# Kernel tuning notes

Hardware: AMD Instinct MI355X
Metric: run time of the kernel (lower is better)

Reference implementation:

```python
import jax, jax.numpy as jnp
import numpy as np

C = 256
LN_EPS = 1e-5
LEAKY_SLOPE = 0.01

def _layernorm(t, g, b):
    mu = jnp.mean(t, axis=-1, keepdims=True)
    var = jnp.mean((t - mu) ** 2, axis=-1, keepdims=True)
    return (t - mu) * jax.lax.rsqrt(var + LN_EPS) * g + b

def setup_inputs() -> dict:
    key = jax.random.key(0)
    ks = jax.random.split(key, 16)
    b, d, h, w = 4, 4096, 64, 64
    s = lambda n: 1.0 / np.sqrt(n)
    return {
        "x": jax.random.normal(ks[0], (b, 1, d), jnp.float32),
        "y": jax.random.normal(ks[1], (b, C, h, w), jnp.float32),
        "q_w": jax.random.normal(ks[2], (C, C), jnp.float32) * s(C),
        "q_b": jnp.zeros((C,), jnp.float32),
        "dw_w": jax.random.normal(ks[3], (C,), jnp.float32),
        "dw_b": jnp.zeros((C,), jnp.float32),
        "kv_w1": jax.random.normal(ks[4], (1, C // 2), jnp.float32),
        "kv_b1": jnp.zeros((C // 2,), jnp.float32),
        "ln1_g": jnp.ones((C // 2,), jnp.float32),
        "ln1_b": jnp.zeros((C // 2,), jnp.float32),
        "kv_w2": jax.random.normal(ks[5], (C // 2, C), jnp.float32) * s(C // 2),
        "kv_b2": jnp.zeros((C,), jnp.float32),
        "ln2_g": jnp.ones((C,), jnp.float32),
        "ln2_b": jnp.zeros((C,), jnp.float32),
        "kv_w3": jax.random.normal(ks[6], (C, C), jnp.float32) * s(C),
        "kv_b3": jnp.zeros((C,), jnp.float32),
        "ln3_g": jnp.ones((C,), jnp.float32),
        "ln3_b": jnp.zeros((C,), jnp.float32),
        "kv_w4": jax.random.normal(ks[7], (C, 2 * C), jnp.float32) * s(C),
        "kv_b4": jnp.zeros((2 * C,), jnp.float32),
        "proj_w": jax.random.normal(ks[8], (C, C), jnp.float32) * s(C),
        "proj_b": jnp.zeros((C,), jnp.float32),
    }

def reference(x, y, q_w, q_b, dw_w, dw_b, kv_w1, kv_b1, ln1_g, ln1_b,
              kv_w2, kv_b2, ln2_g, ln2_b, kv_w3, kv_b3, ln3_g, ln3_b,
              kv_w4, kv_b4, proj_w, proj_b):
    b, c, h, w = y.shape
    # x: [b, 1, d] -> [b, d, 1]; MLP kv-generator lifts each scalar to 2c channels
    t = jnp.swapaxes(x, 1, 2)  # [b, d, 1]
    t = jax.nn.leaky_relu(_layernorm(t @ kv_w1 + kv_b1, ln1_g, ln1_b), LEAKY_SLOPE)
    t = jax.nn.leaky_relu(_layernorm(t @ kv_w2 + kv_b2, ln2_g, ln2_b), LEAKY_SLOPE)
    t = jax.nn.leaky_relu(_layernorm(t @ kv_w3 + kv_b3, ln3_g, ln3_b), LEAKY_SLOPE)
    t = jax.nn.silu(t @ kv_w4 + kv_b4)  # [b, d, 2c]
    k, v = jnp.split(t, 2, axis=-1)  # each [b, d, c]
    k = jnp.swapaxes(k, 1, 2)  # [b, c, d]
    # q = dwconv1x1(conv1x1(y)): 1x1 conv is a channel matmul; depthwise 1x1 is per-channel affine
    q = jnp.einsum('bchw,oc->bohw', y, q_w) + q_b[None, :, None, None]
    q = q * dw_w[None, :, None, None] + dw_b[None, :, None, None]
    q = q.reshape(b, c, h * w).transpose(0, 2, 1)  # [b, hw, c]
    scores = jnp.einsum('bic,bcd->bid', q, k) * (float(c) ** -0.5)  # [b, hw, d]
    attn = jax.nn.softmax(scores, axis=2)
    h_ = jnp.einsum('bid,bdc->bic', attn, v)  # [b, hw, c]
    h_ = h_.transpose(0, 2, 1).reshape(b, c, h, w)
    h_ = jnp.einsum('bchw,oc->bohw', h_, proj_w) + proj_b[None, :, None, None]
    return y + h_
```

## Files before the change

### kernel.cpp

```cpp
#include <hip/hip_runtime.h>
#include <cstdint>
#include <cstddef>

using bf16   = __bf16;
using bf16x8 = __bf16 __attribute__((ext_vector_type(8)));
using f32x4  = float  __attribute__((ext_vector_type(4)));
using u16    = unsigned short;
using ushort8 = __attribute__((ext_vector_type(8))) unsigned short;

#define MFMA16(a, b, c) __builtin_amdgcn_mfma_f32_16x16x32_bf16(a, b, c, 0, 0, 0)

__device__ __forceinline__ u16 f2bf(float f) {
  union { float f; unsigned u; } v; v.f = f;
  unsigned r = v.u + 0x7fffu + ((v.u >> 16) & 1u);
  return (u16)(r >> 16);
}
__device__ __forceinline__ u16 bfc(float f) {
  union { float f; unsigned u; } v; v.f = f;
  return (u16)((v.u + 0x8000u) >> 16);
}
__device__ __forceinline__ float b2f(u16 h) {
  union { unsigned u; float f; } v; v.u = ((unsigned)h) << 16; return v.f;
}
__device__ __forceinline__ bf16x8 ldb8(const u16* p) { return *(const bf16x8*)p; }
__device__ __forceinline__ float red_sum16(float v) {
  v += __shfl_xor(v, 1, 64); v += __shfl_xor(v, 2, 64);
  v += __shfl_xor(v, 4, 64); v += __shfl_xor(v, 8, 64);
  return v;
}
__device__ __forceinline__ void gll16(const u16* g, u16* l) {
  __builtin_amdgcn_global_load_lds(
      (const __attribute__((address_space(1))) void*)g,
      (__attribute__((address_space(3))) void*)l, 16, 0, 0);
}

#define QSCALE 0.09016844005556021f

__global__ void k_prep(const float* __restrict__ kv_w2, const float* __restrict__ kv_w3,
                       const float* __restrict__ kv_w4, const float* __restrict__ q_w,
                       const float* __restrict__ proj_w,
                       u16* __restrict__ Wt2, u16* __restrict__ Wt3, u16* __restrict__ Wt4,
                       u16* __restrict__ Qw, u16* __restrict__ Pww) {
  int idx = blockIdx.x * 256 + threadIdx.x;
  if (idx < 32768) {
    int n = idx >> 7, k = idx & 127;
    Wt2[idx] = f2bf(kv_w2[k * 256 + n]);
  } else if (idx < 98304) {
    int j = idx - 32768, n = j >> 8, k = j & 255;
    Wt3[j] = f2bf(kv_w3[k * 256 + n]);
  } else if (idx < 229376) {
    int j = idx - 98304, n = j >> 8, k = j & 255;
    Wt4[j] = f2bf(kv_w4[k * 512 + n]);
  } else if (idx < 294912) {
    int j = idx - 229376;
    Qw[j] = f2bf(q_w[j]);
  } else if (idx < 360448) {
    int j = idx - 294912;
    Pww[j] = f2bf(proj_w[j]);
  }
}

__device__ __forceinline__ void ln_store(f32x4* acc, const float* __restrict__ bias,
    const float* __restrict__ g, const float* __restrict__ bb, u16* act,
    int w, int quad, int l16) {
  #pragma unroll
  for (int f = 0; f < 16; ++f) {
    float bv = bias[f * 16 + l16];
    acc[f][0] += bv; acc[f][1] += bv; acc[f][2] += bv; acc[f][3] += bv;
  }
  #pragma unroll
  for (int r = 0; r < 4; ++r) {
    float s = 0;
    #pragma unroll
    for (int f = 0; f < 16; ++f) s += acc[f][r];
    s = red_sum16(s);
    float mu = s * (1.f / 256.f);
    float vv = 0;
    #pragma unroll
    for (int f = 0; f < 16; ++f) { float d = acc[f][r] - mu; vv += d * d; }
    vv = red_sum16(vv);
    float inv = rsqrtf(vv * (1.f / 256.f) + 1e-5f);
    int rl = w * 16 + quad * 4 + r;
    #pragma unroll
    for (int f = 0; f < 16; ++f) {
      int col = f * 16 + l16;
      float o = (acc[f][r] - mu) * inv * g[col] + bb[col];
      o = o > 0.f ? o : 0.01f * o;
      act[rl * 264 + col] = f2bf(o);
    }
  }
}

template<int K>
__device__ __forceinline__ void mlp_layer(u16* act, u16* sW, const u16* __restrict__ Wt,
    const float* __restrict__ bias, const float* __restrict__ g, const float* __restrict__ bb,
    int tid, int w, int quad, int l16) {
  bf16x8 af[K / 32];
  #pragma unroll
  for (int kk = 0; kk < K / 32; ++kk) af[kk] = ldb8(act + (w * 16 + l16) * 264 + kk * 32 + quad * 8);
  f32x4 z = {0.f, 0.f, 0.f, 0.f};
  f32x4 acc[16];
  #pragma unroll
  for (int f = 0; f < 16; ++f) acc[f] = z;
  for (int nc = 0; nc < 8; ++nc) {
    __syncthreads();
    #pragma unroll
    for (int p = 0; p < K / 64; ++p) {
      int q = p * 256 + tid; int row = q / (K / 8), c8 = q % (K / 8);
      *(uint4*)(sW + row * 264 + c8 * 8) = *(const uint4*)(Wt + (size_t)(nc * 32 + row) * K + c8 * 8);
    }
    __syncthreads();
    #pragma unroll
    for (int nb = 0; nb < 2; ++nb) {
      int f = nc * 2 + nb;
      #pragma unroll
      for (int kk = 0; kk < K / 32; ++kk)
        acc[f] = MFMA16(af[kk], ldb8(sW + (nb * 16 + l16) * 264 + kk * 32 + quad * 8), acc[f]);
    }
  }
  ln_store(acc, bias, g, bb, act, w, quad, l16);
  __syncthreads();
}

__device__ __forceinline__ void mlp_layer4(u16* act, u16* sW, const u16* __restrict__ Wt4,
    const float* __restrict__ bias4, u16* __restrict__ Kt, u16* __restrict__ Vt,
    int i0, int tid, int w, int quad, int l16) {
  bf16x8 af[8];
  #pragma unroll
  for (int kk = 0; kk < 8; ++kk) af[kk] = ldb8(act + (w * 16 + l16) * 264 + kk * 32 + quad * 8);
  f32x4 z = {0.f, 0.f, 0.f, 0.f};
  for (int h = 0; h < 2; ++h) {
    f32x4 acc[16];
    #pragma unroll
    for (int f = 0; f < 16; ++f) acc[f] = z;
    for (int nc = 0; nc < 8; ++nc) {
      __syncthreads();
      #pragma unroll
      for (int p = 0; p < 4; ++p) {
        int q = p * 256 + tid; int row = q >> 5, c8 = q & 31;
        *(uint4*)(sW + row * 264 + c8 * 8) =
            *(const uint4*)(Wt4 + (size_t)(h * 256 + nc * 32 + row) * 256 + c8 * 8);
      }
      __syncthreads();
      #pragma unroll
      for (int nb = 0; nb < 2; ++nb) {
        int f = nc * 2 + nb;
        #pragma unroll
        for (int kk = 0; kk < 8; ++kk)
          acc[f] = MFMA16(af[kk], ldb8(sW + (nb * 16 + l16) * 264 + kk * 32 + quad * 8), acc[f]);
      }
    }
    #pragma unroll
    for (int f = 0; f < 16; ++f) {
      int col = f * 16 + l16;
      float bv = bias4[h * 256 + col];
      if (h == 0) {
        int chunk = f * 2 + (l16 >> 3), co = col & 7;
        #pragma unroll
        for (int r = 0; r < 4; ++r) {
          int rowg = i0 + w * 16 + quad * 4 + r;
          float v = acc[f][r] + bv;
          v = v / (1.f + __expf(-v));
          int chs = (chunk + (rowg & 31)) & 31;
          Kt[(size_t)rowg * 256 + chs * 8 + co] = f2bf(v);
        }
      } else {
        int rowg0 = i0 + w * 16 + quad * 4;
        int bb2 = rowg0 >> 12, d0 = rowg0 & 4095;
        int dd = d0 & 31, qd = dd >> 3;
        int chs = (qd + (col & 3) + ((col >> 2) & 3)) & 3;
        ushort4 u;
        #pragma unroll
        for (int r = 0; r < 4; ++r) {
          float v = acc[f][r] + bv;
          v = v / (1.f + __expf(-v));
          ((u16*)&u)[r] = f2bf(v);
        }
        size_t off = ((size_t)(bb2 * 128 + (d0 >> 5)) * 8192) + col * 32 + chs * 8 + (dd & 7);
        *(ushort4*)(Vt + off) = u;
      }
    }
  }
}

__global__ __launch_bounds__(256, 2) void k_fused(
    const float* __restrict__ x, const float* __restrict__ w1, const float* __restrict__ bias1,
    const float* __restrict__ g1, const float* __restrict__ bb1,
    const u16* __restrict__ Wt2, const float* __restrict__ bias2,
    const float* __restrict__ g2, const float* __restrict__ bb2,
    const u16* __restrict__ Wt3, const float* __restrict__ bias3,
    const float* __restrict__ g3, const float* __restrict__ bb3,
    const u16* __restrict__ Wt4, const float* __restrict__ bias4,
    const float* __restrict__ y, const u16* __restrict__ Qw,
    const float* __restrict__ qb, const float* __restrict__ dww, const float* __restrict__ dwb,
    u16* __restrict__ Kt, u16* __restrict__ Vt, u16* __restrict__ Qb) {
  __shared__ __align__(16) u16 smem[25344];
  int tid = threadIdx.x, w = tid >> 6, lane = tid & 63, quad = lane >> 4, l16 = lane & 15;

  if (blockIdx.x < 256) {
    u16* act = smem;
    u16* sW  = smem + 16896;
    int i0 = blockIdx.x * 64;
    {
      int rloc = w * 16 + (lane >> 2);
      int c0 = (lane & 3) * 32;
      float xv = x[i0 + rloc];
      float t[32];
      float s = 0.f;
      #pragma unroll
      for (int j = 0; j < 32; ++j) { t[j] = xv * w1[c0 + j] + bias1[c0 + j]; s += t[j]; }
      s += __shfl_xor(s, 1, 64); s += __shfl_xor(s, 2, 64);
      float mu = s * (1.f / 128.f);
      float vv = 0.f;
      #pragma unroll
      for (int j = 0; j < 32; ++j) { float d = t[j] - mu; vv += d * d; }
      vv += __shfl_xor(vv, 1, 64); vv += __shfl_xor(vv, 2, 64);
      float inv = rsqrtf(vv * (1.f / 128.f) + 1e-5f);
      #pragma unroll
      for (int jo = 0; jo < 4; ++jo) {
        ushort8 pk;
        #pragma unroll
        for (int e = 0; e < 8; ++e) {
          int j = jo * 8 + e;
          float o = (t[j] - mu) * inv * g1[c0 + j] + bb1[c0 + j];
          o = o > 0.f ? o : 0.01f * o;
          pk[e] = f2bf(o);
        }
        *(ushort8*)(act + rloc * 264 + c0 + jo * 8) = pk;
      }
    }
    __syncthreads();
    mlp_layer<128>(act, sW, Wt2, bias2, g2, bb2, tid, w, quad, l16);
    mlp_layer<256>(act, sW, Wt3, bias3, g3, bb3, tid, w, quad, l16);
    mlp_layer4(act, sW, Wt4, bias4, Kt, Vt, i0, tid, w, quad, l16);
    return;
  }

  u16* sY = smem;
  u16* sB = smem + 4608;
  int t = blockIdx.x - 256;
  int b = t >> 6, i0 = (t & 63) * 64;
  f32x4 z = {0.f, 0.f, 0.f, 0.f};
  f32x4 acc[16];
  #pragma unroll
  for (int f = 0; f < 16; ++f) acc[f] = z;
  for (int kc = 0; kc < 4; ++kc) {
    if (kc) __syncthreads();
    {
      int cl = tid >> 4;
      int il = (tid & 15) * 4;
      #pragma unroll
      for (int p = 0; p < 4; ++p) {
        int c = kc * 64 + p * 16 + cl;
        float4 v = *(const float4*)(y + ((size_t)(b * 256 + c)) * 4096 + i0 + il);
        sY[(il + 0) * 72 + p * 16 + cl] = f2bf(v.x);
        sY[(il + 1) * 72 + p * 16 + cl] = f2bf(v.y);
        sY[(il + 2) * 72 + p * 16 + cl] = f2bf(v.z);
        sY[(il + 3) * 72 + p * 16 + cl] = f2bf(v.w);
      }
    }
    #pragma unroll
    for (int p = 0; p < 8; ++p) {
      int q = p * 256 + tid; int row = q >> 3, k8 = q & 7;
      *(uint4*)(sB + row * 72 + k8 * 8) = *(const uint4*)(Qw + (size_t)row * 256 + kc * 64 + k8 * 8);
    }
    __syncthreads();
    #pragma unroll
    for (int kk = 0; kk < 2; ++kk) {
      bf16x8 af = ldb8(sY + (w * 16 + l16) * 72 + kk * 32 + quad * 8);
      #pragma unroll
      for (int f = 0; f < 16; ++f) {
        bf16x8 bfr = ldb8(sB + (f * 16 + l16) * 72 + kk * 32 + quad * 8);
        acc[f] = MFMA16(af, bfr, acc[f]);
      }
    }
  }
  #pragma unroll
  for (int f = 0; f < 16; ++f) {
    int col = f * 16 + l16;
    float q0 = qb[col], sc = dww[col], dB = dwb[col];
    #pragma unroll
    for (int r = 0; r < 4; ++r) {
      int rowg = i0 + w * 16 + quad * 4 + r;
      float v = ((acc[f][r] + q0) * sc + dB) * QSCALE;
      Qb[((size_t)(b * 4096 + rowg)) * 256 + col] = f2bf(v);
    }
  }
}

__global__ __launch_bounds__(256, 2) void k_attn(const u16* __restrict__ Qb, const u16* __restrict__ Kt,
    const u16* __restrict__ Vt, u16* __restrict__ Op, float* __restrict__ Ol) {
  __shared__ __align__(16) u16 smem[37888];
  int tid = threadIdx.x, w = tid >> 6, lane = tid & 63, quad = lane >> 4, l16 = lane & 15;
  int b = blockIdx.x & 3, kh = (blockIdx.x >> 2) & 3, qt = blockIdx.x >> 4;
  int i0 = qt * 128 + w * 32;

  bf16x8 qf[2][8];
  {
    const u16* qrow = Qb + ((size_t)(b * 4096 + i0 + l16)) * 256 + quad * 8;
    #pragma unroll
    for (int kk = 0; kk < 8; ++kk) {
      qf[0][kk] = ldb8(qrow + kk * 32);
      qf[1][kk] = ldb8(qrow + 16 * 256 + kk * 32);
    }
  }
  f32x4 z = {0.f, 0.f, 0.f, 0.f};
  f32x4 oacc[2][16];
  #pragma unroll
  for (int sub = 0; sub < 2; ++sub)
    #pragma unroll
    for (int f = 0; f < 16; ++f) oacc[sub][f] = z;
  float l4[2][4] = {{0.f, 0.f, 0.f, 0.f}, {0.f, 0.f, 0.f, 0.f}};

  u16* sPw = smem + 32768 + w * 1280;
  int wp = w & 1;
  const u16* gSrc = ((w < 2) ? Kt : Vt) + ((size_t)(b * 128 + kh * 32) * 8192) + wp * 4096 + lane * 8;
  u16* lBase = smem + ((w < 2) ? 0 : 8192) + wp * 4096 + lane * 8;

  #pragma unroll
  for (int i = 0; i < 8; ++i) gll16(gSrc + i * 512, lBase + i * 512);
  gSrc += 8192;

  #pragma unroll 1
  for (int kt = 0; kt < 32; ++kt) {
    int buf = kt & 1;
    const u16* sK = smem + buf * 16384;
    const u16* sV = sK + 8192;
    asm volatile("s_waitcnt vmcnt(0)" ::: "memory");
    __syncthreads();
    if (kt < 31) {
      u16* dst = lBase + (buf ^ 1) * 16384;
      #pragma unroll
      for (int i = 0; i < 8; ++i) gll16(gSrc + i * 512, dst + i * 512);
      gSrc += 8192;
    }
    f32x4 s00 = z, s01 = z, s10 = z, s11 = z;
    #pragma unroll
    for (int kk = 0; kk < 8; ++kk) {
      int ch0 = (kk * 4 + quad + l16) & 31;
      int ch1 = (ch0 + 16) & 31;
      bf16x8 k0 = ldb8(sK + l16 * 256 + ch0 * 8);
      bf16x8 k1 = ldb8(sK + (16 + l16) * 256 + ch1 * 8);
      s00 = MFMA16(qf[0][kk], k0, s00);
      s01 = MFMA16(qf[0][kk], k1, s01);
      s10 = MFMA16(qf[1][kk], k0, s10);
      s11 = MFMA16(qf[1][kk], k1, s11);
    }
    #pragma unroll
    for (int r = 0; r < 4; ++r) {
      float p0 = exp2f(s00[r]);
      float p1 = exp2f(s01[r]);
      float p2 = exp2f(s10[r]);
      float p3 = exp2f(s11[r]);
      l4[0][r] += p0 + p1;
      l4[1][r] += p2 + p3;
      int row0 = (quad * 4 + r) * 40;
      sPw[row0 + l16]            = bfc(p0);
      sPw[row0 + 16 + l16]       = bfc(p1);
      sPw[640 + row0 + l16]      = bfc(p2);
      sPw[640 + row0 + 16 + l16] = bfc(p3);
    }
    asm volatile("s_waitcnt lgkmcnt(0)" ::: "memory");
    bf16x8 pf0 = ldb8(sPw + l16 * 40 + quad * 8);
    bf16x8 pf1 = ldb8(sPw + 640 + l16 * 40 + quad * 8);
    #pragma unroll
    for (int f = 0; f < 16; ++f) {
      int c = f * 16 + l16;
      int chs = (quad + (c & 3) + ((c >> 2) & 3)) & 3;
      bf16x8 vf = ldb8(sV + c * 32 + chs * 8);
      oacc[0][f] = MFMA16(pf0, vf, oacc[0][f]);
      oacc[1][f] = MFMA16(pf1, vf, oacc[1][f]);
    }
  }
  #pragma unroll
  for (int sub = 0; sub < 2; ++sub)
    #pragma unroll
    for (int r = 0; r < 4; ++r) l4[sub][r] = red_sum16(l4[sub][r]);
  #pragma unroll
  for (int sub = 0; sub < 2; ++sub)
    #pragma unroll
    for (int r = 0; r < 4; ++r) {
      size_t gr = (size_t)kh * 16384 + b * 4096 + i0 + sub * 16 + quad * 4 + r;
      u16* orow = Op + gr * 256;
      #pragma unroll
      for (int f = 0; f < 16; ++f) orow[f * 16 + l16] = f2bf(oacc[sub][f][r]);
      if (l16 == 0) Ol[gr] = l4[sub][r];
    }
}

__global__ __launch_bounds__(256) void k_proj(const u16* __restrict__ Op, const float* __restrict__ Ol,
    const u16* __restrict__ Pw, const float* __restrict__ pb, const float* __restrict__ y,
    float* __restrict__ out) {
  __shared__ u16 sA[64 * 136];
  __shared__ u16 sB[64 * 136];
  __shared__ float sW[64];
  int tid = threadIdx.x, w = tid >> 6, lane = tid & 63, quad = lane >> 4, l16 = lane & 15;
  int i0 = blockIdx.x * 64, o0 = blockIdx.y * 64, b = blockIdx.z;
  if (tid < 64) {
    size_t gr = (size_t)b * 4096 + i0 + tid;
    float L = Ol[gr] + Ol[gr + 16384] + Ol[gr + 32768] + Ol[gr + 49152];
    sW[tid] = 1.f / L;
  }
  __syncthreads();
  f32x4 z = {0.f, 0.f, 0.f, 0.f};
  f32x4 acc[4] = {z, z, z, z};
  for (int kc = 0; kc < 2; ++kc) {
    if (kc) __syncthreads();
    #pragma unroll
    for (int p = 0; p < 4; ++p) {
      int q = p * 256 + tid; int row = q >> 4, c8 = q & 15;
      *(uint4*)(sA + row * 136 + c8 * 8) = *(const uint4*)(Pw + ((size_t)(o0 + row)) * 256 + kc * 128 + c8 * 8);
      size_t gr = (size_t)b * 4096 + i0 + row;
      const u16* hp = Op + gr * 256 + kc * 128 + c8 * 8;
      uint4 u0 = *(const uint4*)(hp);
      uint4 u1 = *(const uint4*)(hp + 4194304);
      uint4 u2 = *(const uint4*)(hp + 8388608);
      uint4 u3 = *(const uint4*)(hp + 12582912);
      float wr = sW[row];
      const u16* p0 = (const u16*)&u0; const u16* p1 = (const u16*)&u1;
      const u16* p2 = (const u16*)&u2; const u16* p3 = (const u16*)&u3;
      ushort8 ov;
      #pragma unroll
      for (int e = 0; e < 8; ++e) {
        float v = (b2f(p0[e]) + b2f(p1[e]) + b2f(p2[e]) + b2f(p3[e])) * wr;
        ov[e] = f2bf(v);
      }
      *(ushort8*)(sB + row * 136 + c8 * 8) = ov;
    }
    __syncthreads();
    #pragma unroll
    for (int kk = 0; kk < 4; ++kk) {
      bf16x8 af = ldb8(sA + (w * 16 + l16) * 136 + kk * 32 + quad * 8);
      #pragma unroll
      for (int nb = 0; nb < 4; ++nb) {
        bf16x8 bfr = ldb8(sB + (nb * 16 + l16) * 136 + kk * 32 + quad * 8);
        acc[nb] = MFMA16(af, bfr, acc[nb]);
      }
    }
  }
  #pragma unroll
  for (int nb = 0; nb < 4; ++nb) {
    #pragma unroll
    for (int r = 0; r < 4; ++r) {
      int og = o0 + w * 16 + quad * 4 + r;
      size_t idx = ((size_t)(b * 256 + og)) * 4096 + i0 + nb * 16 + l16;
      out[idx] = y[idx] + acc[nb][r] + pb[og];
    }
  }
}

extern "C" void kernel_launch(void* const* d_in, const int* in_sizes, int n_in,
                              void* d_out, int out_size, void* d_ws, size_t ws_size,
                              hipStream_t stream) {
  (void)in_sizes; (void)n_in; (void)out_size; (void)ws_size;
  const float* x     = (const float*)d_in[0];
  const float* y     = (const float*)d_in[1];
  const float* q_w   = (const float*)d_in[2];
  const float* q_b   = (const float*)d_in[3];
  const float* dw_w  = (const float*)d_in[4];
  const float* dw_b  = (const float*)d_in[5];
  const float* kv_w1 = (const float*)d_in[6];
  const float* kv_b1 = (const float*)d_in[7];
  const float* ln1_g = (const float*)d_in[8];
  const float* ln1_b = (const float*)d_in[9];
  const float* kv_w2 = (const float*)d_in[10];
  const float* kv_b2 = (const float*)d_in[11];
  const float* ln2_g = (const float*)d_in[12];
  const float* ln2_b = (const float*)d_in[13];
  const float* kv_w3 = (const float*)d_in[14];
  const float* kv_b3 = (const float*)d_in[15];
  const float* ln3_g = (const float*)d_in[16];
  const float* ln3_b = (const float*)d_in[17];
  const float* kv_w4 = (const float*)d_in[18];
  const float* kv_b4 = (const float*)d_in[19];
  const float* proj_w = (const float*)d_in[20];
  const float* proj_b = (const float*)d_in[21];
  float* out = (float*)d_out;
  unsigned char* ws = (unsigned char*)d_ws;

  u16* Wt2 = (u16*)(ws + 0);
  u16* Wt3 = (u16*)(ws + 65536);
  u16* Wt4 = (u16*)(ws + 196608);
  u16* Qw  = (u16*)(ws + 458752);
  u16* Pww = (u16*)(ws + 589824);
  u16* Qb  = (u16*)(ws + 9437184);
  u16* Kt  = (u16*)(ws + 17825792);
  u16* Vt  = (u16*)(ws + 26214400);
  u16* Op  = (u16*)(ws + 34603008);
  float* Ol = (float*)(ws + 68157440);

  k_prep<<<1408, 256, 0, stream>>>(kv_w2, kv_w3, kv_w4, q_w, proj_w, Wt2, Wt3, Wt4, Qw, Pww);
  k_fused<<<512, 256, 0, stream>>>(x, kv_w1, kv_b1, ln1_g, ln1_b,
                                   Wt2, kv_b2, ln2_g, ln2_b,
                                   Wt3, kv_b3, ln3_g, ln3_b,
                                   Wt4, kv_b4,
                                   y, Qw, q_b, dw_w, dw_b,
                                   Kt, Vt, Qb);
  k_attn<<<512, 256, 0, stream>>>(Qb, Kt, Vt, Op, Ol);
  k_proj<<<dim3(64, 4, 4), 256, 0, stream>>>(Op, Ol, Pww, proj_b, y, out);
}
```

Measured before the change: 269.1 us.

## Make KV-MLP layers wave-local with direct global weight loads; pad P staging

The KV-generator MLP in k_fused now gives each wave its own 16-row activation tile in LDS and reads weight fragments straight from global memory (L2-cached) into MFMA operands. This removes the block-wide __syncthreads and the cooperative LDS staging of weight chunks. The row-level LayerNorm reductions are remapped to match. Separately, the attention kernel's P staging buffer gets a per-row skew to reduce LDS bank conflicts. The trade-off is more global and L2 weight traffic per wave and higher load latency in exchange for no barriers.

```diff
diff --git a/kernel.cpp b/kernel.cpp
--- a/kernel.cpp
+++ b/kernel.cpp
@@ -60,9 +60,24 @@
   }
 }
 
-__device__ __forceinline__ void ln_store(f32x4* acc, const float* __restrict__ bias,
-    const float* __restrict__ g, const float* __restrict__ bb, u16* act,
-    int w, int quad, int l16) {
+template<int K>
+__device__ __forceinline__ void wave_layer(u16* act, const u16* __restrict__ Wt,
+    const float* __restrict__ bias, const float* __restrict__ g, const float* __restrict__ bb,
+    int quad, int l16) {
+  bf16x8 af[K / 32];
+  #pragma unroll
+  for (int kk = 0; kk < K / 32; ++kk) af[kk] = ldb8(act + l16 * 264 + kk * 32 + quad * 8);
+  f32x4 z = {0.f, 0.f, 0.f, 0.f};
+  f32x4 acc[16];
+  #pragma unroll
+  for (int f = 0; f < 16; ++f) acc[f] = z;
+  #pragma unroll
+  for (int nb = 0; nb < 16; ++nb) {
+    const u16* wrow = Wt + (size_t)(nb * 16 + l16) * K + quad * 8;
+    #pragma unroll
+    for (int kk = 0; kk < K / 32; ++kk)
+      acc[nb] = MFMA16(af[kk], ldb8(wrow + kk * 32), acc[nb]);
+  }
   #pragma unroll
   for (int f = 0; f < 16; ++f) {
     float bv = bias[f * 16 + l16];
@@ -80,7 +95,7 @@
     for (int f = 0; f < 16; ++f) { float d = acc[f][r] - mu; vv += d * d; }
     vv = red_sum16(vv);
     float inv = rsqrtf(vv * (1.f / 256.f) + 1e-5f);
-    int rl = w * 16 + quad * 4 + r;
+    int rl = quad * 4 + r;
     #pragma unroll
     for (int f = 0; f < 16; ++f) {
       int col = f * 16 + l16;
@@ -89,98 +104,7 @@
       act[rl * 264 + col] = f2bf(o);
     }
   }
-}
-
-template<int K>
-__device__ __forceinline__ void mlp_layer(u16* act, u16* sW, const u16* __restrict__ Wt,
-    const float* __restrict__ bias, const float* __restrict__ g, const float* __restrict__ bb,
-    int tid, int w, int quad, int l16) {
-  bf16x8 af[K / 32];
-  #pragma unroll
-  for (int kk = 0; kk < K / 32; ++kk) af[kk] = ldb8(act + (w * 16 + l16) * 264 + kk * 32 + quad * 8);
-  f32x4 z = {0.f, 0.f, 0.f, 0.f};
-  f32x4 acc[16];
-  #pragma unroll
-  for (int f = 0; f < 16; ++f) acc[f] = z;
-  for (int nc = 0; nc < 8; ++nc) {
-    __syncthreads();
-    #pragma unroll
-    for (int p = 0; p < K / 64; ++p) {
-      int q = p * 256 + tid; int row = q / (K / 8), c8 = q % (K / 8);
-      *(uint4*)(sW + row * 264 + c8 * 8) = *(const uint4*)(Wt + (size_t)(nc * 32 + row) * K + c8 * 8);
-    }
-    __syncthreads();
-    #pragma unroll
-    for (int nb = 0; nb < 2; ++nb) {
-      int f = nc * 2 + nb;
-      #pragma unroll
-      for (int kk = 0; kk < K / 32; ++kk)
-        acc[f] = MFMA16(af[kk], ldb8(sW + (nb * 16 + l16) * 264 + kk * 32 + quad * 8), acc[f]);
-    }
-  }
-  ln_store(acc, bias, g, bb, act, w, quad, l16);
-  __syncthreads();
-}
-
-__device__ __forceinline__ void mlp_layer4(u16* act, u16* sW, const u16* __restrict__ Wt4,
-    const float* __restrict__ bias4, u16* __restrict__ Kt, u16* __restrict__ Vt,
-    int i0, int tid, int w, int quad, int l16) {
-  bf16x8 af[8];
-  #pragma unroll
-  for (int kk = 0; kk < 8; ++kk) af[kk] = ldb8(act + (w * 16 + l16) * 264 + kk * 32 + quad * 8);
-  f32x4 z = {0.f, 0.f, 0.f, 0.f};
-  for (int h = 0; h < 2; ++h) {
-    f32x4 acc[16];
-    #pragma unroll
-    for (int f = 0; f < 16; ++f) acc[f] = z;
-    for (int nc = 0; nc < 8; ++nc) {
-      __syncthreads();
-      #pragma unroll
-      for (int p = 0; p < 4; ++p) {
-        int q = p * 256 + tid; int row = q >> 5, c8 = q & 31;
-        *(uint4*)(sW + row * 264 + c8 * 8) =
-            *(const uint4*)(Wt4 + (size_t)(h * 256 + nc * 32 + row) * 256 + c8 * 8);
-      }
-      __syncthreads();
-      #pragma unroll
-      for (int nb = 0; nb < 2; ++nb) {
-        int f = nc * 2 + nb;
-        #pragma unroll
-        for (int kk = 0; kk < 8; ++kk)
-          acc[f] = MFMA16(af[kk], ldb8(sW + (nb * 16 + l16) * 264 + kk * 32 + quad * 8), acc[f]);
-      }
-    }
-    #pragma unroll
-    for (int f = 0; f < 16; ++f) {
-      int col = f * 16 + l16;
-      float bv = bias4[h * 256 + col];
-      if (h == 0) {
-        int chunk = f * 2 + (l16 >> 3), co = col & 7;
-        #pragma unroll
-        for (int r = 0; r < 4; ++r) {
-          int rowg = i0 + w * 16 + quad * 4 + r;
-          float v = acc[f][r] + bv;
-          v = v / (1.f + __expf(-v));
-          int chs = (chunk + (rowg & 31)) & 31;
-          Kt[(size_t)rowg * 256 + chs * 8 + co] = f2bf(v);
-        }
-      } else {
-        int rowg0 = i0 + w * 16 + quad * 4;
-        int bb2 = rowg0 >> 12, d0 = rowg0 & 4095;
-        int dd = d0 & 31, qd = dd >> 3;
-        int chs = (qd + (col & 3) + ((col >> 2) & 3)) & 3;
-        ushort4 u;
-        #pragma unroll
-        for (int r = 0; r < 4; ++r) {
-          float v = acc[f][r] + bv;
-          v = v / (1.f + __expf(-v));
-          ((u16*)&u)[r] = f2bf(v);
-        }
-        size_t off = ((size_t)(bb2 * 128 + (d0 >> 5)) * 8192) + col * 32 + chs * 8 + (dd & 7);
-        *(ushort4*)(Vt + off) = u;
-      }
-    }
-  }
+  asm volatile("s_waitcnt lgkmcnt(0)" ::: "memory");
 }
 
 __global__ __launch_bounds__(256, 2) void k_fused(
@@ -194,27 +118,26 @@
     const float* __restrict__ y, const u16* __restrict__ Qw,
     const float* __restrict__ qb, const float* __restrict__ dww, const float* __restrict__ dwb,
     u16* __restrict__ Kt, u16* __restrict__ Vt, u16* __restrict__ Qb) {
-  __shared__ __align__(16) u16 smem[25344];
+  __shared__ __align__(16) u16 smem[23040];
   int tid = threadIdx.x, w = tid >> 6, lane = tid & 63, quad = lane >> 4, l16 = lane & 15;
 
   if (blockIdx.x < 256) {
-    u16* act = smem;
-    u16* sW  = smem + 16896;
-    int i0 = blockIdx.x * 64;
+    u16* act = smem + w * 4224;
+    int i0b = blockIdx.x * 64;
+    int rbase = i0b + w * 16;
     {
-      int rloc = w * 16 + (lane >> 2);
-      int c0 = (lane & 3) * 32;
-      float xv = x[i0 + rloc];
+      int c0 = quad * 32;
+      float xv = x[rbase + l16];
       float t[32];
       float s = 0.f;
       #pragma unroll
       for (int j = 0; j < 32; ++j) { t[j] = xv * w1[c0 + j] + bias1[c0 + j]; s += t[j]; }
-      s += __shfl_xor(s, 1, 64); s += __shfl_xor(s, 2, 64);
+      s += __shfl_xor(s, 16, 64); s += __shfl_xor(s, 32, 64);
       float mu = s * (1.f / 128.f);
       float vv = 0.f;
       #pragma unroll
       for (int j = 0; j < 32; ++j) { float d = t[j] - mu; vv += d * d; }
-      vv += __shfl_xor(vv, 1, 64); vv += __shfl_xor(vv, 2, 64);
+      vv += __shfl_xor(vv, 16, 64); vv += __shfl_xor(vv, 32, 64);
       float inv = rsqrtf(vv * (1.f / 128.f) + 1e-5f);
       #pragma unroll
       for (int jo = 0; jo < 4; ++jo) {
@@ -226,13 +149,60 @@
           o = o > 0.f ? o : 0.01f * o;
           pk[e] = f2bf(o);
         }
-        *(ushort8*)(act + rloc * 264 + c0 + jo * 8) = pk;
-      }
-    }
-    __syncthreads();
-    mlp_layer<128>(act, sW, Wt2, bias2, g2, bb2, tid, w, quad, l16);
-    mlp_layer<256>(act, sW, Wt3, bias3, g3, bb3, tid, w, quad, l16);
-    mlp_layer4(act, sW, Wt4, bias4, Kt, Vt, i0, tid, w, quad, l16);
+        *(ushort8*)(act + l16 * 264 + c0 + jo * 8) = pk;
+      }
+    }
+    asm volatile("s_waitcnt lgkmcnt(0)" ::: "memory");
+    wave_layer<128>(act, Wt2, bias2, g2, bb2, quad, l16);
+    wave_layer<256>(act, Wt3, bias3, g3, bb3, quad, l16);
+    {
+      bf16x8 af[8];
+      #pragma unroll
+      for (int kk = 0; kk < 8; ++kk) af[kk] = ldb8(act + l16 * 264 + kk * 32 + quad * 8);
+      f32x4 z = {0.f, 0.f, 0.f, 0.f};
+      for (int h = 0; h < 2; ++h) {
+        f32x4 acc[16];
+        #pragma unroll
+        for (int f = 0; f < 16; ++f) acc[f] = z;
+        #pragma unroll
+        for (int nb = 0; nb < 16; ++nb) {
+          const u16* wrow = Wt4 + (size_t)(h * 256 + nb * 16 + l16) * 256 + quad * 8;
+          #pragma unroll
+          for (int kk = 0; kk < 8; ++kk)
+            acc[nb] = MFMA16(af[kk], ldb8(wrow + kk * 32), acc[nb]);
+        }
+        #pragma unroll
+        for (int f = 0; f < 16; ++f) {
+          int col = f * 16 + l16;
+          float bv = bias4[h * 256 + col];
+          if (h == 0) {
+            int chunk = f * 2 + (l16 >> 3), co = col & 7;
+            #pragma unroll
+            for (int r = 0; r < 4; ++r) {
+              int rowg = rbase + quad * 4 + r;
+              float v = acc[f][r] + bv;
+              v = v / (1.f + __expf(-v));
+              int chs = (chunk + (rowg & 31)) & 31;
+              Kt[(size_t)rowg * 256 + chs * 8 + co] = f2bf(v);
+            }
+          } else {
+            int rowg0 = rbase + quad * 4;
+            int bb2_ = rowg0 >> 12, d0 = rowg0 & 4095;
+            int dd = d0 & 31, qd = dd >> 3;
+            int chs = (qd + (col & 3) + ((col >> 2) & 3)) & 3;
+            ushort4 u;
+            #pragma unroll
+            for (int r = 0; r < 4; ++r) {
+              float v = acc[f][r] + bv;
+              v = v / (1.f + __expf(-v));
+              ((u16*)&u)[r] = f2bf(v);
+            }
+            size_t off = ((size_t)(bb2_ * 128 + (d0 >> 5)) * 8192) + col * 32 + chs * 8 + (dd & 7);
+            *(ushort4*)(Vt + off) = u;
+          }
+        }
+      }
+    }
     return;
   }
 
@@ -290,7 +260,7 @@
 
 __global__ __launch_bounds__(256, 2) void k_attn(const u16* __restrict__ Qb, const u16* __restrict__ Kt,
     const u16* __restrict__ Vt, u16* __restrict__ Op, float* __restrict__ Ol) {
-  __shared__ __align__(16) u16 smem[37888];
+  __shared__ __align__(16) u16 smem[38144];
   int tid = threadIdx.x, w = tid >> 6, lane = tid & 63, quad = lane >> 4, l16 = lane & 15;
   int b = blockIdx.x & 3, kh = (blockIdx.x >> 2) & 3, qt = blockIdx.x >> 4;
   int i0 = qt * 128 + w * 32;
@@ -312,7 +282,7 @@
     for (int f = 0; f < 16; ++f) oacc[sub][f] = z;
   float l4[2][4] = {{0.f, 0.f, 0.f, 0.f}, {0.f, 0.f, 0.f, 0.f}};
 
-  u16* sPw = smem + 32768 + w * 1280;
+  u16* sPw = smem + 32768 + w * 1344;
   int wp = w & 1;
   const u16* gSrc = ((w < 2) ? Kt : Vt) + ((size_t)(b * 128 + kh * 32) * 8192) + wp * 4096 + lane * 8;
   u16* lBase = smem + ((w < 2) ? 0 : 8192) + wp * 4096 + lane * 8;
@@ -354,15 +324,16 @@
       float p3 = exp2f(s11[r]);
       l4[0][r] += p0 + p1;
       l4[1][r] += p2 + p3;
-      int row0 = (quad * 4 + r) * 40;
-      sPw[row0 + l16]            = bfc(p0);
-      sPw[row0 + 16 + l16]       = bfc(p1);
-      sPw[640 + row0 + l16]      = bfc(p2);
-      sPw[640 + row0 + 16 + l16] = bfc(p3);
+      int row0 = (quad * 4 + r) * 40 + quad * 8;
+      sPw[row0 + l16]             = bfc(p0);
+      sPw[row0 + 16 + l16]        = bfc(p1);
+      sPw[672 + row0 + l16]       = bfc(p2);
+      sPw[672 + row0 + 16 + l16]  = bfc(p3);
     }
     asm volatile("s_waitcnt lgkmcnt(0)" ::: "memory");
-    bf16x8 pf0 = ldb8(sPw + l16 * 40 + quad * 8);
-    bf16x8 pf1 = ldb8(sPw + 640 + l16 * 40 + quad * 8);
+    int prow = l16 * 40 + (l16 >> 2) * 8 + quad * 8;
+    bf16x8 pf0 = ldb8(sPw + prow);
+    bf16x8 pf1 = ldb8(sPw + 672 + prow);
     #pragma unroll
     for (int f = 0; f < 16; ++f) {
       int c = f * 16 + l16;
```

New measurement: 299.3 us. 1.11x slower.
